# Optimization experiments

Measured on AMD Instinct MI355X. Metric: run time of the kernel, lower is better.

The kernel has to match this reference:

```python
import jax, jax.numpy as jnp
import numpy as np

N_NODES = 100000
N_EDGES = 1600000
N_GRAPHS = 64
N_TYPES = 17   # len(TYPES)
D = 128        # embedding_dim == hidden_dim
H = 128
O = 128


def setup_inputs() -> dict:
    key = jax.random.key(0)
    ks = jax.random.split(key, 8)
    node_ids = jax.random.randint(ks[0], (N_NODES,), 0, N_TYPES)
    edge_index = jax.random.randint(ks[1], (2, N_EDGES), 0, N_NODES)
    batch = jnp.sort(jax.random.randint(ks[2], (N_NODES,), 0, N_GRAPHS))
    emb_table = jax.random.normal(ks[3], (N_TYPES, D), dtype=jnp.float32)
    W1 = jax.random.normal(ks[4], (D, H), dtype=jnp.float32) * (1.0 / np.sqrt(D))
    b1 = jnp.zeros((H,), dtype=jnp.float32)
    W2 = jax.random.normal(ks[5], (H, O), dtype=jnp.float32) * (1.0 / np.sqrt(H))
    b2 = jnp.zeros((O,), dtype=jnp.float32)
    return {"node_ids": node_ids, "edge_index": edge_index, "batch": batch,
            "num_graphs": N_GRAPHS, "emb_table": emb_table,
            "W1": W1, "b1": b1, "W2": W2, "b2": b2}


def _gcn_conv(x, W, b, src, dst, n_nodes):
    # PyG GCNConv: h = x W; symmetric norm with self-loops (src/dst already include them);
    # out[i] = sum_{e: dst_e=i} norm_e * h[src_e] + b
    h = x @ W
    deg = jax.ops.segment_sum(jnp.ones_like(dst, dtype=h.dtype), dst,
                              num_segments=n_nodes)
    dinv = jnp.where(deg > 0, jax.lax.rsqrt(deg), 0.0)
    norm = dinv[src] * dinv[dst]                      # [E+N]
    msgs = h[src] * norm[:, None]                     # [E+N, out_dim]
    return jax.ops.segment_sum(msgs, dst, num_segments=n_nodes) + b


def reference(node_ids, edge_index, batch, num_graphs, emb_table, W1, b1, W2, b2):
    n = node_ids.shape[0]
    loops = jnp.arange(n, dtype=edge_index.dtype)
    src = jnp.concatenate([edge_index[0], loops])
    dst = jnp.concatenate([edge_index[1], loops])

    x = emb_table[node_ids]                            # embedding lookup [N, D]
    x = _gcn_conv(x, W1, b1, src, dst, n)
    x = jax.nn.relu(x)
    # F.dropout(training=self.training) is identity in eval mode
    x = _gcn_conv(x, W2, b2, src, dst, n)

    # global_mean_pool over batch index
    sums = jax.ops.segment_sum(x, batch, num_segments=num_graphs)   # [G, O]
    cnts = jax.ops.segment_sum(jnp.ones((n,), dtype=x.dtype), batch,
                               num_segments=num_graphs)
    return sums / jnp.maximum(cnts, 1.0)[:, None]
```

## Files before the change

### kernel.cpp

```cpp
#include <hip/hip_runtime.h>
#include <hip/hip_bf16.h>


#define DDIM 128
#define GMAX 64
#define BPG  8
#define NBK  (GMAX * BPG)
#define NPB  2048
#define SLICES 32
#define MAXGN 2048
typedef unsigned int uint;
typedef unsigned short ushort;
typedef float v2f __attribute__((ext_vector_type(2)));

__global__ void k_gb2(const int* __restrict__ batch, int N,
                      int* __restrict__ gBound, int* __restrict__ bkBound) {
    __shared__ int gB[GMAX + 1];
    int t = threadIdx.x;
    if (t <= GMAX) {
        int key = t, lo = 0, hi = N;
        while (lo < hi) {
            int mid = (lo + hi) >> 1;
            if (batch[mid] < key) lo = mid + 1; else hi = mid;
        }
        gB[t] = lo;
        gBound[t] = lo;
    }
    __syncthreads();
    for (int bk = t; bk <= NBK; bk += 256) {
        int v;
        if (bk == NBK) v = gB[GMAX];
        else {
            int g = bk >> 3, s = bk & 7;
            int A = gB[g], L = gB[g + 1] - A;
            v = A + (int)((long long)L * s / BPG);
        }
        bkBound[bk] = v;
    }
}

__device__ __forceinline__ int bksearch(const int* bkB, int idx) {
    int lo = 0, hi = NBK - 1;
#pragma unroll
    for (int it = 0; it < 9; it++) {
        int mid = (lo + hi + 1) >> 1;
        if (bkB[mid] <= idx) lo = mid; else hi = mid - 1;
    }
    return lo;
}

__global__ void __launch_bounds__(256) k_p1(
        const int* __restrict__ dst, const int* __restrict__ bkBound,
        int* __restrict__ blockHist, int E) {
    __shared__ int h[NBK];
    __shared__ int bkB[NBK + 1];
    int t = threadIdx.x;
    for (int k = t; k < NBK; k += 256) h[k] = 0;
    for (int k = t; k <= NBK; k += 256) bkB[k] = bkBound[k];
    __syncthreads();
    int per = (E + NPB - 1) / NPB;
    int lo = blockIdx.x * per;
    int hi = lo + per; if (hi > E) hi = E;
    for (int cb = lo; cb < hi; cb += 1024) {
        int idx_[4]; bool v_[4];
#pragma unroll
        for (int q = 0; q < 4; q++) {
            int item = cb + q * 256 + t;
            v_[q] = item < hi;
            idx_[q] = v_[q] ? dst[item] : 0;
        }
#pragma unroll
        for (int q = 0; q < 4; q++)
            if (v_[q]) atomicAdd(&h[bksearch(bkB, idx_[q])], 1);
    }
    __syncthreads();
    for (int k = t; k < NBK; k += 256) blockHist[blockIdx.x * NBK + k] = h[k];
}

__global__ void __launch_bounds__(256) k_scanG(
        const int* __restrict__ blockHist, int* __restrict__ localBase,
        int* __restrict__ tot) {
    __shared__ int sm[256];
    int g = blockIdx.x, t = threadIdx.x;
    const int PER = NPB / 256;
    int v[PER], loc[PER];
    int run = 0;
#pragma unroll
    for (int q = 0; q < PER; q++) {
        v[q] = blockHist[(t * PER + q) * NBK + g];
        loc[q] = run;
        run += v[q];
    }
    sm[t] = run; __syncthreads();
    for (int off = 1; off < 256; off <<= 1) {
        int a = (t >= off) ? sm[t - off] : 0;
        __syncthreads();
        sm[t] += a; __syncthreads();
    }
    int excl = sm[t] - run;
#pragma unroll
    for (int q = 0; q < PER; q++)
        localBase[(t * PER + q) * NBK + g] = excl + loc[q];
    if (t == 255) tot[g] = sm[255];
}

__global__ void __launch_bounds__(256) k_scanT(
        const int* __restrict__ tot, int* __restrict__ bkStart) {
    __shared__ int sm[256];
    int t = threadIdx.x;
    int v0 = tot[2 * t], v1 = tot[2 * t + 1];
    int run = v0 + v1;
    sm[t] = run; __syncthreads();
    for (int off = 1; off < 256; off <<= 1) {
        int a = (t >= off) ? sm[t - off] : 0;
        __syncthreads();
        sm[t] += a; __syncthreads();
    }
    int excl = sm[t] - run;
    bkStart[2 * t] = excl;
    bkStart[2 * t + 1] = excl + v0;
    if (t == 255) bkStart[NBK] = sm[255];
}

__global__ void __launch_bounds__(256) k_part(
        const int* __restrict__ src, const int* __restrict__ dst,
        const int* __restrict__ bkBound, const int* __restrict__ localBase,
        const int* __restrict__ bkStart, uint* __restrict__ partsKey, int E) {
    __shared__ int rk[NBK];
    __shared__ int runOff[NBK];
    __shared__ int base[NBK];
    __shared__ int bkB[NBK + 1];
    __shared__ uint sbuf[1024];
    __shared__ ushort sb2[1024];
    __shared__ int sms[256];
    int t = threadIdx.x, b = blockIdx.x;
    for (int k = t; k < NBK; k += 256) base[k] = bkStart[k] + localBase[b * NBK + k];
    for (int k = t; k <= NBK; k += 256) bkB[k] = bkBound[k];
    int per = (E + NPB - 1) / NPB;
    int lo = b * per;
    int hi = lo + per; if (hi > E) hi = E;
    for (int cb = lo; cb < hi; cb += 1024) {
        int cnt = hi - cb; if (cnt > 1024) cnt = 1024;
        for (int k = t; k < NBK; k += 256) rk[k] = 0;
        __syncthreads();
        uint key_[4]; int bk_[4], r_[4]; bool v_[4];
#pragma unroll
        for (int q = 0; q < 4; q++) {
            int item = cb + q * 256 + t;
            v_[q] = item < hi;
            key_[q] = 0; bk_[q] = 0; r_[q] = 0;
            if (v_[q]) {
                int s = src[item], d = dst[item];
                int bk = bksearch(bkB, d);
                bk_[q] = bk;
                int dLG = d - bkB[(bk >> 3) << 3];
                key_[q] = ((uint)dLG << 17) | (uint)s;
            }
        }
#pragma unroll
        for (int q = 0; q < 4; q++)
            if (v_[q]) r_[q] = atomicAdd(&rk[bk_[q]], 1);
        __syncthreads();
        {
            int v0 = rk[2 * t], v1 = rk[2 * t + 1];
            int run = v0 + v1;
            sms[t] = run; __syncthreads();
            for (int off = 1; off < 256; off <<= 1) {
                int a = (t >= off) ? sms[t - off] : 0;
                __syncthreads();
                sms[t] += a; __syncthreads();
            }
            int excl = sms[t] - run;
            runOff[2 * t] = excl;
            runOff[2 * t + 1] = excl + v0;
        }
        __syncthreads();
#pragma unroll
        for (int q = 0; q < 4; q++)
            if (v_[q]) {
                int p = runOff[bk_[q]] + r_[q];
                sbuf[p] = key_[q];
                sb2[p] = (ushort)bk_[q];
            }
        __syncthreads();
#pragma unroll
        for (int q = 0; q < 4; q++) {
            int p = q * 256 + t;
            if (p < cnt) {
                int bk = sb2[p];
                partsKey[base[bk] + (p - runOff[bk])] = sbuf[p];
            }
        }
        __syncthreads();
        for (int k = t; k < NBK; k += 256) base[k] += rk[k];
        __syncthreads();
    }
}

__global__ void __launch_bounds__(256) k_cnt2(
        const uint* __restrict__ partsKey, const int* __restrict__ bkBound,
        const int* __restrict__ bkStart, const int* __restrict__ ids,
        float2* __restrict__ nd) {
    __shared__ int cnt[256];
    int b = blockIdx.x, t = threadIdx.x;
    cnt[t] = 0;
    __syncthreads();
    int nodeLo = bkBound[b];
    int gOff = nodeLo - bkBound[(b >> 3) << 3];
    int lo = bkStart[b], hi = bkStart[b + 1];
    for (int idx = lo + t; idx < hi; idx += 256) {
        uint key = partsKey[idx];
        int dL = (int)((key >> 17) & 0xFFF) - gOff;
        atomicAdd(&cnt[dL], 1);
    }
    __syncthreads();
    int nn = bkBound[b + 1] - nodeLo;
    if (t < nn) {
        int i = nodeLo + t;
        nd[i] = make_float2(rsqrtf((float)(cnt[t] + 1)),
                            __int_as_float(ids[i]));
    }
}

__global__ void k_t1(const float* __restrict__ emb, const float* __restrict__ W1,
                     float* __restrict__ t1) {
    int t = blockIdx.x, f = threadIdx.x;
    float acc = 0.f;
    for (int k = 0; k < DDIM; k++) acc += emb[t * DDIM + k] * W1[k * DDIM + f];
    t1[t * DDIM + f] = acc;
}

__global__ void __launch_bounds__(256) k_x1b(
        const uint* __restrict__ partsKey, const int* __restrict__ bkBound,
        const int* __restrict__ bkStart, const float2* __restrict__ nd,
        const float* __restrict__ t1, const float* __restrict__ b1,
        ushort* __restrict__ z, float* __restrict__ poolY) {
    __shared__ float t1s[17 * DDIM];
    __shared__ float CL[256 * 17];
    __shared__ float2 ndL[256];
    __shared__ float bL[DDIM];
    __shared__ float redS[4][DDIM];
    int b = blockIdx.x, t = threadIdx.x;
    int nodeLo = bkBound[b], nn = bkBound[b + 1] - nodeLo;
    int gOff = nodeLo - bkBound[(b >> 3) << 3];
    for (int k = t; k < 17 * DDIM; k += 256) t1s[k] = t1[k];
    for (int k = t; k < 256 * 17; k += 256) CL[k] = 0.f;
    if (t < DDIM) bL[t] = b1[t];
    if (t < nn) ndL[t] = nd[nodeLo + t];
    __syncthreads();
    int lo = bkStart[b], hi = bkStart[b + 1];
    for (int cb = lo; cb < hi; cb += 2048) {
        uint key_[8]; bool v_[8];
#pragma unroll
        for (int q = 0; q < 8; q++) {
            int idx = cb + q * 256 + t;
            v_[q] = idx < hi;
            key_[q] = v_[q] ? partsKey[idx] : 0u;
        }
#pragma unroll
        for (int q = 0; q < 8; q++) {
            if (v_[q]) {
                uint key = key_[q];
                int s = key & 0x1FFFF;
                int dL = (int)((key >> 17) & 0xFFF) - gOff;
                float2 ns = nd[s];
                atomicAdd(&CL[dL * 17 + __float_as_int(ns.y)], ns.x);
            }
        }
    }
    __syncthreads();
    int lane = t & 63, wave = t >> 6;
    float sx = 0.f, sy = 0.f;
    for (int n = wave; n < nn; n += 4) {
        float dinv = ndL[n].x;
        int ti = __float_as_int(ndL[n].y);
        float ax = dinv * t1s[ti * DDIM + lane];
        float ay = dinv * t1s[ti * DDIM + 64 + lane];
#pragma unroll
        for (int tt = 0; tt < 17; tt++) {
            float c = CL[n * 17 + tt];
            ax += c * t1s[tt * DDIM + lane];
            ay += c * t1s[tt * DDIM + 64 + lane];
        }
        float vx = bL[lane]      + dinv * ax;
        float vy = bL[64 + lane] + dinv * ay;
        vx = vx > 0.f ? vx : 0.f;
        vy = vy > 0.f ? vy : 0.f;
        int pk = __builtin_amdgcn_cvt_pk_fp8_f32(dinv * vx, dinv * vy, 0, false);
        z[(size_t)(nodeLo + n) * 64 + lane] = (ushort)(pk & 0xFFFF);
        float d2 = dinv * dinv;
        sx += d2 * vx;
        sy += d2 * vy;
    }
    redS[wave][lane] = sx;
    redS[wave][64 + lane] = sy;
    __syncthreads();
    if (wave == 0) {
        int g = b >> 3;
        float vx = redS[0][lane] + redS[1][lane] + redS[2][lane] + redS[3][lane];
        float vy = redS[0][64 + lane] + redS[1][64 + lane]
                 + redS[2][64 + lane] + redS[3][64 + lane];
        atomicAdd(&poolY[g * DDIM + lane], vx);
        atomicAdd(&poolY[g * DDIM + 64 + lane], vy);
    }
}

__global__ void __launch_bounds__(256) k_conv2g(
        const uint* __restrict__ partsKey, const int* __restrict__ bkStart,
        const int* __restrict__ gBound, const float2* __restrict__ nd,
        const ushort* __restrict__ z, float* __restrict__ poolY) {
    __shared__ float dinvG[MAXGN];
    __shared__ uint  mk[4][64];
    __shared__ float red[4][DDIM];
    int t = threadIdx.x, lane = t & 63, wave = t >> 6;
    int b = blockIdx.x;
    int j = b >> 3;
    int g = (b & 7) * 8 + (j >> 5);
    int sl = j & 31;
    int nLo = gBound[g], nn = gBound[g + 1] - nLo;
    for (int k = t; k < nn; k += 256) dinvG[k] = nd[nLo + k].x;
    if (t == 0) dinvG[MAXGN - 1] = 0.f;
    __syncthreads();
    int a = bkStart[g * BPG], bnd = bkStart[(g + 1) * BPG];
    long long len = bnd - a;
    int s0 = a + (int)(len * sl / SLICES);
    int s1 = a + (int)(len * (sl + 1) / SLICES);
    const uint SENT = (uint)(MAXGN - 1) << 17;
    float ax = 0.f, ay = 0.f;
    for (int cb = s0 + wave * 64; cb < s1; cb += 4 * 64) {
        int idx = cb + lane;
        mk[wave][lane] = (idx < s1) ? partsKey[idx] : SENT;
#pragma unroll
        for (int jj = 0; jj < 64; jj += 16) {
            uint kk[16]; uint vv[16];
#pragma unroll
            for (int k = 0; k < 16; k++) kk[k] = mk[wave][jj + k];
#pragma unroll
            for (int k = 0; k < 16; k++)
                vv[k] = (uint)z[(size_t)(kk[k] & 0x1FFFF) * 64 + lane];
#pragma unroll
            for (int k = 0; k < 16; k++) {
                float w = dinvG[(kk[k] >> 17) & 0xFFF];
                v2f f = __builtin_amdgcn_cvt_pk_f32_fp8((int)vv[k], false);
                ax += w * f.x;
                ay += w * f.y;
            }
        }
    }
    red[wave][lane] = ax;
    red[wave][64 + lane] = ay;
    __syncthreads();
    if (wave == 0) {
        float vx = red[0][lane] + red[1][lane] + red[2][lane] + red[3][lane];
        float vy = red[0][64 + lane] + red[1][64 + lane] + red[2][64 + lane] + red[3][64 + lane];
        atomicAdd(&poolY[g * DDIM + lane], vx);
        atomicAdd(&poolY[g * DDIM + 64 + lane], vy);
    }
}

__global__ void __launch_bounds__(128) k_out(
        const float* __restrict__ poolY, const int* __restrict__ gBound,
        const float* __restrict__ W2, const float* __restrict__ b2,
        float* __restrict__ out) {
    __shared__ float py[DDIM];
    int g = blockIdx.x, f = threadIdx.x;
    py[f] = poolY[g * DDIM + f];
    __syncthreads();
    float acc = 0.f;
    for (int k = 0; k < DDIM; k++) acc += py[k] * W2[k * DDIM + f];
    int c = gBound[g + 1] - gBound[g];
    out[g * DDIM + f] = (c > 0) ? (b2[f] + acc / (float)c) : 0.f;
}

extern "C" void kernel_launch(void* const* d_in, const int* in_sizes, int n_in,
                              void* d_out, int out_size, void* d_ws, size_t ws_size,
                              hipStream_t stream) {
    const int* node_ids = (const int*)d_in[0];
    const int* edge_index = (const int*)d_in[1];
    const int* batch = (const int*)d_in[2];
    const float* emb = (const float*)d_in[4];
    const float* W1 = (const float*)d_in[5];
    const float* b1 = (const float*)d_in[6];
    const float* W2 = (const float*)d_in[7];
    const float* b2 = (const float*)d_in[8];
    float* out = (float*)d_out;

    const int N = in_sizes[0];
    const int E = in_sizes[1] / 2;
    const int* src = edge_index;
    const int* dst = edge_index + E;

    char* ws = (char*)d_ws;
    size_t off = 0;
    auto carve = [&](size_t bytes) { char* p = ws + off; off = (off + bytes + 255) & ~size_t(255); return p; };
    ushort* z         = (ushort*)carve((size_t)N * 64 * 2);
    uint*   partsKey  = (uint*)carve((size_t)E * 4);
    float2* nd        = (float2*)carve((size_t)N * 8);
    int*    blockHist = (int*)carve((size_t)NPB * NBK * 4);
    int*    localBase = (int*)carve((size_t)NPB * NBK * 4);
    int*    tot       = (int*)carve(NBK * 4);
    int*    bkStart   = (int*)carve((NBK + 1) * 4);
    int*    gBound    = (int*)carve((GMAX + 1) * 4);
    int*    bkBound   = (int*)carve((NBK + 1) * 4);
    float*  t1        = (float*)carve(17 * DDIM * 4);
    float*  poolY     = (float*)carve((size_t)GMAX * DDIM * 4);

    hipMemsetAsync(poolY, 0, (size_t)GMAX * DDIM * 4, stream);

    k_gb2<<<1, 256, 0, stream>>>(batch, N, gBound, bkBound);
    k_p1<<<NPB, 256, 0, stream>>>(dst, bkBound, blockHist, E);
    k_scanG<<<NBK, 256, 0, stream>>>(blockHist, localBase, tot);
    k_scanT<<<1, 256, 0, stream>>>(tot, bkStart);
    k_part<<<NPB, 256, 0, stream>>>(src, dst, bkBound, localBase, bkStart,
                                    partsKey, E);
    k_cnt2<<<NBK, 256, 0, stream>>>(partsKey, bkBound, bkStart, node_ids, nd);
    k_t1<<<17, DDIM, 0, stream>>>(emb, W1, t1);
    k_x1b<<<NBK, 256, 0, stream>>>(partsKey, bkBound, bkStart, nd, t1, b1, z, poolY);
    k_conv2g<<<GMAX * SLICES, 256, 0, stream>>>(partsKey, bkStart, gBound, nd, z, poolY);
    k_out<<<GMAX, 128, 0, stream>>>(poolY, gBound, W2, b2, out);
}
```

Before: 205.0 us.

## Split z into feature-quarter planes and quadruple conv2 grid; vectorize edge loads

```diff
diff --git a/kernel.cpp b/kernel.cpp
--- a/kernel.cpp
+++ b/kernel.cpp
@@ -13,29 +13,41 @@
 typedef unsigned short ushort;
 typedef float v2f __attribute__((ext_vector_type(2)));
 
-__global__ void k_gb2(const int* __restrict__ batch, int N,
-                      int* __restrict__ gBound, int* __restrict__ bkBound) {
-    __shared__ int gB[GMAX + 1];
-    int t = threadIdx.x;
-    if (t <= GMAX) {
-        int key = t, lo = 0, hi = N;
-        while (lo < hi) {
-            int mid = (lo + hi) >> 1;
-            if (batch[mid] < key) lo = mid + 1; else hi = mid;
-        }
-        gB[t] = lo;
-        gBound[t] = lo;
-    }
-    __syncthreads();
-    for (int bk = t; bk <= NBK; bk += 256) {
-        int v;
-        if (bk == NBK) v = gB[GMAX];
-        else {
-            int g = bk >> 3, s = bk & 7;
-            int A = gB[g], L = gB[g + 1] - A;
-            v = A + (int)((long long)L * s / BPG);
-        }
-        bkBound[bk] = v;
+__global__ void __launch_bounds__(256) k_setup(
+        const int* __restrict__ batch, int N,
+        int* __restrict__ gBound, int* __restrict__ bkBound,
+        const float* __restrict__ emb, const float* __restrict__ W1,
+        float* __restrict__ t1) {
+    int t = threadIdx.x, b = blockIdx.x;
+    if (b == 0) {
+        __shared__ int gB[GMAX + 1];
+        if (t <= GMAX) {
+            int key = t, lo = 0, hi = N;
+            while (lo < hi) {
+                int mid = (lo + hi) >> 1;
+                if (batch[mid] < key) lo = mid + 1; else hi = mid;
+            }
+            gB[t] = lo;
+            gBound[t] = lo;
+        }
+        __syncthreads();
+        for (int bk = t; bk <= NBK; bk += 256) {
+            int v;
+            if (bk == NBK) v = gB[GMAX];
+            else {
+                int g = bk >> 3, s = bk & 7;
+                int A = gB[g], L = gB[g + 1] - A;
+                v = A + (int)((long long)L * s / BPG);
+            }
+            bkBound[bk] = v;
+        }
+    } else {
+        int row = b - 1;
+        if (t < DDIM) {
+            float acc = 0.f;
+            for (int k = 0; k < DDIM; k++) acc += emb[row * DDIM + k] * W1[k * DDIM + t];
+            t1[row * DDIM + t] = acc;
+        }
     }
 }
 
@@ -47,6 +59,13 @@
         if (bkB[mid] <= idx) lo = mid; else hi = mid - 1;
     }
     return lo;
+}
+
+__device__ __forceinline__ void blockRange(int E, int b, int& lo, int& hi) {
+    int per = ((E + NPB - 1) / NPB + 3) & ~3;
+    lo = b * per;
+    hi = lo + per; if (hi > E) hi = E;
+    if (lo > E) lo = E;
 }
 
 __global__ void __launch_bounds__(256) k_p1(
@@ -58,20 +77,21 @@
     for (int k = t; k < NBK; k += 256) h[k] = 0;
     for (int k = t; k <= NBK; k += 256) bkB[k] = bkBound[k];
     __syncthreads();
-    int per = (E + NPB - 1) / NPB;
-    int lo = blockIdx.x * per;
-    int hi = lo + per; if (hi > E) hi = E;
+    int lo, hi; blockRange(E, blockIdx.x, lo, hi);
     for (int cb = lo; cb < hi; cb += 1024) {
-        int idx_[4]; bool v_[4];
-#pragma unroll
-        for (int q = 0; q < 4; q++) {
-            int item = cb + q * 256 + t;
-            v_[q] = item < hi;
-            idx_[q] = v_[q] ? dst[item] : 0;
-        }
-#pragma unroll
-        for (int q = 0; q < 4; q++)
-            if (v_[q]) atomicAdd(&h[bksearch(bkB, idx_[q])], 1);
+        if (cb + 1024 <= hi) {
+            int4 d4 = *(const int4*)(dst + cb + t * 4);
+            atomicAdd(&h[bksearch(bkB, d4.x)], 1);
+            atomicAdd(&h[bksearch(bkB, d4.y)], 1);
+            atomicAdd(&h[bksearch(bkB, d4.z)], 1);
+            atomicAdd(&h[bksearch(bkB, d4.w)], 1);
+        } else {
+#pragma unroll
+            for (int q = 0; q < 4; q++) {
+                int item = cb + q * 256 + t;
+                if (item < hi) atomicAdd(&h[bksearch(bkB, dst[item])], 1);
+            }
+        }
     }
     __syncthreads();
     for (int k = t; k < NBK; k += 256) blockHist[blockIdx.x * NBK + k] = h[k];
@@ -136,25 +156,38 @@
     int t = threadIdx.x, b = blockIdx.x;
     for (int k = t; k < NBK; k += 256) base[k] = bkStart[k] + localBase[b * NBK + k];
     for (int k = t; k <= NBK; k += 256) bkB[k] = bkBound[k];
-    int per = (E + NPB - 1) / NPB;
-    int lo = b * per;
-    int hi = lo + per; if (hi > E) hi = E;
+    int lo, hi; blockRange(E, b, lo, hi);
     for (int cb = lo; cb < hi; cb += 1024) {
         int cnt = hi - cb; if (cnt > 1024) cnt = 1024;
         for (int k = t; k < NBK; k += 256) rk[k] = 0;
         __syncthreads();
         uint key_[4]; int bk_[4], r_[4]; bool v_[4];
-#pragma unroll
-        for (int q = 0; q < 4; q++) {
-            int item = cb + q * 256 + t;
-            v_[q] = item < hi;
-            key_[q] = 0; bk_[q] = 0; r_[q] = 0;
-            if (v_[q]) {
-                int s = src[item], d = dst[item];
-                int bk = bksearch(bkB, d);
+        if (cb + 1024 <= hi) {
+            int4 s4 = *(const int4*)(src + cb + t * 4);
+            int4 d4 = *(const int4*)(dst + cb + t * 4);
+            int ss[4] = {s4.x, s4.y, s4.z, s4.w};
+            int dd[4] = {d4.x, d4.y, d4.z, d4.w};
+#pragma unroll
+            for (int q = 0; q < 4; q++) {
+                v_[q] = true;
+                int bk = bksearch(bkB, dd[q]);
                 bk_[q] = bk;
-                int dLG = d - bkB[(bk >> 3) << 3];
-                key_[q] = ((uint)dLG << 17) | (uint)s;
+                int dLG = dd[q] - bkB[(bk >> 3) << 3];
+                key_[q] = ((uint)dLG << 17) | (uint)ss[q];
+            }
+        } else {
+#pragma unroll
+            for (int q = 0; q < 4; q++) {
+                int item = cb + q * 256 + t;
+                v_[q] = item < hi;
+                key_[q] = 0; bk_[q] = 0;
+                if (v_[q]) {
+                    int s = src[item], d = dst[item];
+                    int bk = bksearch(bkB, d);
+                    bk_[q] = bk;
+                    int dLG = d - bkB[(bk >> 3) << 3];
+                    key_[q] = ((uint)dLG << 17) | (uint)s;
+                }
             }
         }
 #pragma unroll
@@ -200,7 +233,7 @@
 __global__ void __launch_bounds__(256) k_cnt2(
         const uint* __restrict__ partsKey, const int* __restrict__ bkBound,
         const int* __restrict__ bkStart, const int* __restrict__ ids,
-        float2* __restrict__ nd) {
+        float2* __restrict__ nd, float* __restrict__ dinvA) {
     __shared__ int cnt[256];
     int b = blockIdx.x, t = threadIdx.x;
     cnt[t] = 0;
@@ -217,24 +250,17 @@
     int nn = bkBound[b + 1] - nodeLo;
     if (t < nn) {
         int i = nodeLo + t;
-        nd[i] = make_float2(rsqrtf((float)(cnt[t] + 1)),
-                            __int_as_float(ids[i]));
-    }
-}
-
-__global__ void k_t1(const float* __restrict__ emb, const float* __restrict__ W1,
-                     float* __restrict__ t1) {
-    int t = blockIdx.x, f = threadIdx.x;
-    float acc = 0.f;
-    for (int k = 0; k < DDIM; k++) acc += emb[t * DDIM + k] * W1[k * DDIM + f];
-    t1[t * DDIM + f] = acc;
+        float dinv = rsqrtf((float)(cnt[t] + 1));
+        nd[i] = make_float2(dinv, __int_as_float(ids[i]));
+        dinvA[i] = dinv;
+    }
 }
 
 __global__ void __launch_bounds__(256) k_x1b(
         const uint* __restrict__ partsKey, const int* __restrict__ bkBound,
         const int* __restrict__ bkStart, const float2* __restrict__ nd,
         const float* __restrict__ t1, const float* __restrict__ b1,
-        ushort* __restrict__ z, float* __restrict__ poolY) {
+        ushort* __restrict__ z4, float* __restrict__ poolY, int N) {
     __shared__ float t1s[17 * DDIM];
     __shared__ float CL[256 * 17];
     __shared__ float2 ndL[256];
@@ -270,6 +296,7 @@
     }
     __syncthreads();
     int lane = t & 63, wave = t >> 6;
+    int f4 = lane >> 4, u = lane & 15;
     float sx = 0.f, sy = 0.f;
     for (int n = wave; n < nn; n += 4) {
         float dinv = ndL[n].x;
@@ -287,7 +314,7 @@
         vx = vx > 0.f ? vx : 0.f;
         vy = vy > 0.f ? vy : 0.f;
         int pk = __builtin_amdgcn_cvt_pk_fp8_f32(dinv * vx, dinv * vy, 0, false);
-        z[(size_t)(nodeLo + n) * 64 + lane] = (ushort)(pk & 0xFFFF);
+        z4[(size_t)f4 * N * 16 + (size_t)(nodeLo + n) * 16 + u] = (ushort)(pk & 0xFFFF);
         float d2 = dinv * dinv;
         sx += d2 * vx;
         sy += d2 * vy;
@@ -307,18 +334,19 @@
 
 __global__ void __launch_bounds__(256) k_conv2g(
         const uint* __restrict__ partsKey, const int* __restrict__ bkStart,
-        const int* __restrict__ gBound, const float2* __restrict__ nd,
-        const ushort* __restrict__ z, float* __restrict__ poolY) {
+        const int* __restrict__ gBound, const float* __restrict__ dinvA,
+        const ushort* __restrict__ z4, float* __restrict__ poolY, int N) {
     __shared__ float dinvG[MAXGN];
     __shared__ uint  mk[4][64];
-    __shared__ float red[4][DDIM];
+    __shared__ float redx[4][64];
+    __shared__ float redy[4][64];
     int t = threadIdx.x, lane = t & 63, wave = t >> 6;
     int b = blockIdx.x;
-    int j = b >> 3;
-    int g = (b & 7) * 8 + (j >> 5);
-    int sl = j & 31;
+    int fs = (b & 7) >> 1;
+    int idx2 = (b >> 3) + (b & 1) * 1024;
+    int g = idx2 >> 5, sl = idx2 & 31;
     int nLo = gBound[g], nn = gBound[g + 1] - nLo;
-    for (int k = t; k < nn; k += 256) dinvG[k] = nd[nLo + k].x;
+    for (int k = t; k < nn; k += 256) dinvG[k] = dinvA[nLo + k];
     if (t == 0) dinvG[MAXGN - 1] = 0.f;
     __syncthreads();
     int a = bkStart[g * BPG], bnd = bkStart[(g + 1) * BPG];
@@ -326,35 +354,36 @@
     int s0 = a + (int)(len * sl / SLICES);
     int s1 = a + (int)(len * (sl + 1) / SLICES);
     const uint SENT = (uint)(MAXGN - 1) << 17;
+    const ushort* zs = z4 + (size_t)fs * N * 16;
+    int isub = lane >> 4, u = lane & 15;
     float ax = 0.f, ay = 0.f;
     for (int cb = s0 + wave * 64; cb < s1; cb += 4 * 64) {
         int idx = cb + lane;
         mk[wave][lane] = (idx < s1) ? partsKey[idx] : SENT;
 #pragma unroll
-        for (int jj = 0; jj < 64; jj += 16) {
-            uint kk[16]; uint vv[16];
-#pragma unroll
-            for (int k = 0; k < 16; k++) kk[k] = mk[wave][jj + k];
-#pragma unroll
-            for (int k = 0; k < 16; k++)
-                vv[k] = (uint)z[(size_t)(kk[k] & 0x1FFFF) * 64 + lane];
-#pragma unroll
-            for (int k = 0; k < 16; k++) {
-                float w = dinvG[(kk[k] >> 17) & 0xFFF];
-                v2f f = __builtin_amdgcn_cvt_pk_f32_fp8((int)vv[k], false);
-                ax += w * f.x;
-                ay += w * f.y;
-            }
-        }
-    }
-    red[wave][lane] = ax;
-    red[wave][64 + lane] = ay;
-    __syncthreads();
-    if (wave == 0) {
-        float vx = red[0][lane] + red[1][lane] + red[2][lane] + red[3][lane];
-        float vy = red[0][64 + lane] + red[1][64 + lane] + red[2][64 + lane] + red[3][64 + lane];
-        atomicAdd(&poolY[g * DDIM + lane], vx);
-        atomicAdd(&poolY[g * DDIM + 64 + lane], vy);
+        for (int st = 0; st < 16; st++) {
+            uint key = mk[wave][st * 4 + isub];
+            uint v = (uint)zs[(size_t)(key & 0x1FFFF) * 16 + u];
+            float w = dinvG[(key >> 17) & 0xFFF];
+            v2f f = __builtin_amdgcn_cvt_pk_f32_fp8((int)v, false);
+            ax += w * f.x;
+            ay += w * f.y;
+        }
+    }
+    redx[wave][lane] = ax;
+    redy[wave][lane] = ay;
+    __syncthreads();
+    if (t < 16) {
+        float sx = 0.f, sy = 0.f;
+#pragma unroll
+        for (int w = 0; w < 4; w++)
+#pragma unroll
+            for (int is = 0; is < 4; is++) {
+                sx += redx[w][is * 16 + t];
+                sy += redy[w][is * 16 + t];
+            }
+        atomicAdd(&poolY[g * DDIM + fs * 16 + t], sx);
+        atomicAdd(&poolY[g * DDIM + 64 + fs * 16 + t], sy);
     }
 }
 
@@ -393,9 +422,10 @@
     char* ws = (char*)d_ws;
     size_t off = 0;
     auto carve = [&](size_t bytes) { char* p = ws + off; off = (off + bytes + 255) & ~size_t(255); return p; };
-    ushort* z         = (ushort*)carve((size_t)N * 64 * 2);
+    ushort* z4        = (ushort*)carve((size_t)N * 64 * 2);
     uint*   partsKey  = (uint*)carve((size_t)E * 4);
     float2* nd        = (float2*)carve((size_t)N * 8);
+    float*  dinvA     = (float*)carve((size_t)N * 4);
     int*    blockHist = (int*)carve((size_t)NPB * NBK * 4);
     int*    localBase = (int*)carve((size_t)NPB * NBK * 4);
     int*    tot       = (int*)carve(NBK * 4);
@@ -407,15 +437,16 @@
 
     hipMemsetAsync(poolY, 0, (size_t)GMAX * DDIM * 4, stream);
 
-    k_gb2<<<1, 256, 0, stream>>>(batch, N, gBound, bkBound);
+    k_setup<<<18, 256, 0, stream>>>(batch, N, gBound, bkBound, emb, W1, t1);
     k_p1<<<NPB, 256, 0, stream>>>(dst, bkBound, blockHist, E);
     k_scanG<<<NBK, 256, 0, stream>>>(blockHist, localBase, tot);
     k_scanT<<<1, 256, 0, stream>>>(tot, bkStart);
     k_part<<<NPB, 256, 0, stream>>>(src, dst, bkBound, localBase, bkStart,
                                     partsKey, E);
-    k_cnt2<<<NBK, 256, 0, stream>>>(partsKey, bkBound, bkStart, node_ids, nd);
-    k_t1<<<17, DDIM, 0, stream>>>(emb, W1, t1);
-    k_x1b<<<NBK, 256, 0, stream>>>(partsKey, bkBound, bkStart, nd, t1, b1, z, poolY);
-    k_conv2g<<<GMAX * SLICES, 256, 0, stream>>>(partsKey, bkStart, gBound, nd, z, poolY);
+    k_cnt2<<<NBK, 256, 0, stream>>>(partsKey, bkBound, bkStart, node_ids, nd, dinvA);
+    k_x1b<<<NBK, 256, 0, stream>>>(partsKey, bkBound, bkStart, nd, t1, b1,
+                                   z4, poolY, N);
+    k_conv2g<<<GMAX * SLICES * 4, 256, 0, stream>>>(partsKey, bkStart, gBound,
+                                                    dinvA, z4, poolY, N);
     k_out<<<GMAX, 128, 0, stream>>>(poolY, gBound, W2, b2, out);
 }
```

Result: slower. 210.8 us (+2.8%).
